# Performance work log

Measured on AMD Instinct MI355X. Metric: run time of the kernel, lower is better.

## Reference

```python
import jax, jax.numpy as jnp
import numpy as np

N = 50000
E = 800000
IN = 256
C = 64  # hidden_channels
H = 4   # heads
NEG_SLOPE = 0.2


def _rand(key, shape, scale=0.05):
    return jax.random.normal(key, shape, dtype=jnp.float32) * scale


def setup_inputs() -> dict:
    key = jax.random.key(0)
    ks = jax.random.split(key, 32)
    inp = {
        'x': jax.random.normal(ks[0], (N, IN), dtype=jnp.float32),
        'edge_index': jax.random.randint(ks[1], (2, E), 0, N, dtype=jnp.int64),
        'edge_attr': jax.random.uniform(ks[2], (E, 1), dtype=jnp.float32),
    }
    ki = 3
    for l, din in zip((1, 2, 3), (IN, C, C)):
        inp[f'Wl{l}'] = _rand(ks[ki + 0], (din, H * C))
        inp[f'bl{l}'] = jnp.zeros((H * C,), jnp.float32)
        inp[f'Wr{l}'] = _rand(ks[ki + 1], (din, H * C))
        inp[f'br{l}'] = jnp.zeros((H * C,), jnp.float32)
        inp[f'We{l}'] = _rand(ks[ki + 2], (1, H * C))
        inp[f'att{l}'] = _rand(ks[ki + 3], (H, C))
        inp[f'bias{l}'] = jnp.zeros((C,), jnp.float32)
        ki += 4
    inp['prelu_w'] = jnp.full((C,), 0.25, jnp.float32)  # nn.PReLU default init
    return inp


def gatv2_layer(x, src, dst, eattr, Wl, bl, Wr, br, We, att, bias, n):
    h, c = att.shape
    xl = (x @ Wl + bl).reshape(n, h, c)   # source transform
    xr = (x @ Wr + br).reshape(n, h, c)   # destination transform
    ee = (eattr @ We).reshape(-1, h, c)   # edge-feature transform
    m = xl[src] + xr[dst] + ee            # [E', H, C] per-edge messages
    score = jnp.sum(jax.nn.leaky_relu(m, NEG_SLOPE) * att, axis=-1)  # [E', H]
    # segment softmax over destination node neighborhoods (PyG softmax, eps=1e-16)
    mx = jax.ops.segment_max(score, dst, num_segments=n)
    mx = jnp.where(jnp.isfinite(mx), mx, 0.0)
    ex = jnp.exp(score - mx[dst])
    den = jax.ops.segment_sum(ex, dst, num_segments=n)
    alpha = ex / (den[dst] + 1e-16)
    out = jax.ops.segment_sum(alpha[:, :, None] * xl[src], dst, num_segments=n)
    return out.mean(axis=1) + bias        # concat=False -> head mean, then bias


def reference(x, edge_index, edge_attr,
              Wl1, bl1, Wr1, br1, We1, att1, bias1,
              Wl2, bl2, Wr2, br2, We2, att2, bias2,
              Wl3, bl3, Wr3, br3, We3, att3, bias3,
              prelu_w):
    src, dst = edge_index[0], edge_index[1]
    n = x.shape[0]
    # add_self_loops with fill_value='mean': self-loop attr = mean of incoming edge_attr
    cnt = jax.ops.segment_sum(jnp.ones((src.shape[0],), jnp.float32), dst, num_segments=n)
    loop_attr = jax.ops.segment_sum(edge_attr, dst, num_segments=n) / jnp.maximum(cnt, 1.0)[:, None]
    loops = jnp.arange(n, dtype=src.dtype)
    src2 = jnp.concatenate([src, loops])
    dst2 = jnp.concatenate([dst, loops])
    ea2 = jnp.concatenate([edge_attr, loop_attr], axis=0)

    h = gatv2_layer(x, src2, dst2, ea2, Wl1, bl1, Wr1, br1, We1, att1, bias1, n)
    h = gatv2_layer(h, src2, dst2, ea2, Wl2, bl2, Wr2, br2, We2, att2, bias2, n)
    h = gatv2_layer(h, src2, dst2, ea2, Wl3, bl3, Wr3, br3, We3, att3, bias3, n)
    return jnp.where(h >= 0, h, prelu_w * h)  # PReLU per-channel
```

## Files before the change

### kernel.cpp

```cpp
#include <hip/hip_runtime.h>

#define HC 256
#define CCH 64
#define NEG 0.2f

__device__ __forceinline__ float lk(float m) { return m > 0.f ? m : NEG * m; }


__global__ void deg_kernel(const int* __restrict__ dst,
                           const float* __restrict__ eattr,
                           int* __restrict__ cnt, float* __restrict__ sumf, int E) {
  int e = blockIdx.x * blockDim.x + threadIdx.x;
  if (e >= E) return;
  int d = dst[e];
  atomicAdd(&cnt[d], 1);
  atomicAdd(&sumf[d], eattr[e]);
}

__global__ void scan_kernel(const int* __restrict__ cnt, const float* __restrict__ sumf,
                            int* __restrict__ rowptr, float* __restrict__ loopat, int n) {
  __shared__ int wsum[16];
  __shared__ int carry_s;
  int tid = threadIdx.x, lane = tid & 63, w = tid >> 6;
  if (tid == 0) carry_s = 0;
  __syncthreads();
  for (int base = 0; base < n; base += 1024) {
    int i = base + tid;
    int v = (i < n) ? cnt[i] : 0;
    int s = v;
    #pragma unroll
    for (int off = 1; off < 64; off <<= 1) {
      int t = __shfl_up(s, off, 64);
      if (lane >= off) s += t;
    }
    if (lane == 63) wsum[w] = s;
    __syncthreads();
    int woff = 0;
    for (int j = 0; j < w; j++) woff += wsum[j];
    int excl = carry_s + woff + s - v;
    if (i < n) {
      rowptr[i] = excl;
      loopat[i] = sumf[i] / fmaxf((float)v, 1.0f);
    }
    __syncthreads();
    if (tid == 1023) carry_s = excl + v;
    __syncthreads();
  }
  if (threadIdx.x == 0) rowptr[n] = carry_s;
}

__global__ void csr_fill_kernel(const int* __restrict__ src,
                                const int* __restrict__ dst,
                                const float* __restrict__ eattr,
                                const int* __restrict__ rowptr,
                                int* __restrict__ fill,
                                int* __restrict__ csr_src, float* __restrict__ csr_ea, int E) {
  int e = blockIdx.x * blockDim.x + threadIdx.x;
  if (e >= E) return;
  int d = dst[e];
  int p = atomicAdd(&fill[d], 1);
  int slot = rowptr[d] + p;
  csr_src[slot] = src[e];
  csr_ea[slot] = eattr[e];
}


__global__ __launch_bounds__(256)
void gemm_dual(const float* __restrict__ A,
               const float* __restrict__ Wl, const float* __restrict__ bl,
               const float* __restrict__ Wr, const float* __restrict__ br,
               float* __restrict__ xl, float* __restrict__ xr,
               int nrows, int K) {
  __shared__ float As[16][132];
  __shared__ float Ws[16][64];
  const float* W; const float* bb; float* out; int bn;
  if (blockIdx.x < 4) { W = Wl; bb = bl; out = xl; bn = blockIdx.x * 64; }
  else                { W = Wr; bb = br; out = xr; bn = (blockIdx.x - 4) * 64; }
  int bm = blockIdx.y * 128;
  int tx = threadIdx.x & 15;
  int ty = threadIdx.x >> 4;
  int arow = threadIdx.x & 127;
  int akk  = (threadIdx.x >> 7) * 8;
  int wkk  = threadIdx.x >> 4;
  int wc4  = (threadIdx.x & 15) * 4;
  float acc[8][4] = {};
  int row0 = bm + arow;
  for (int k0 = 0; k0 < K; k0 += 16) {
    float4 a0 = make_float4(0.f,0.f,0.f,0.f), a1 = a0;
    if (row0 < nrows) {
      const float* ap = A + (size_t)row0 * K + k0 + akk;
      a0 = *(const float4*)ap;
      a1 = *(const float4*)(ap + 4);
    }
    As[akk+0][arow] = a0.x; As[akk+1][arow] = a0.y;
    As[akk+2][arow] = a0.z; As[akk+3][arow] = a0.w;
    As[akk+4][arow] = a1.x; As[akk+5][arow] = a1.y;
    As[akk+6][arow] = a1.z; As[akk+7][arow] = a1.w;
    *(float4*)&Ws[wkk][wc4] = *(const float4*)(W + (size_t)(k0 + wkk) * HC + bn + wc4);
    __syncthreads();
    #pragma unroll
    for (int k = 0; k < 16; k++) {
      float av[8], wv[4];
      *(float4*)&av[0] = *(const float4*)&As[k][ty * 8];
      *(float4*)&av[4] = *(const float4*)&As[k][ty * 8 + 4];
      *(float4*)&wv[0] = *(const float4*)&Ws[k][tx * 4];
      #pragma unroll
      for (int i = 0; i < 8; i++)
        #pragma unroll
        for (int j = 0; j < 4; j++)
          acc[i][j] = fmaf(av[i], wv[j], acc[i][j]);
    }
    __syncthreads();
  }
  float4 bv = *(const float4*)(bb + bn + tx * 4);
  #pragma unroll
  for (int i = 0; i < 8; i++) {
    int row = bm + ty * 8 + i;
    if (row < nrows) {
      float4 o;
      o.x = acc[i][0] + bv.x;
      o.y = acc[i][1] + bv.y;
      o.z = acc[i][2] + bv.z;
      o.w = acc[i][3] + bv.w;
      *(float4*)(out + (size_t)row * HC + bn + tx * 4) = o;
    }
  }
}


template<int B>
__device__ __forceinline__ void proc_edges(
    const float* __restrict__ xl, int i,
    const int* __restrict__ csr_src, const float* __restrict__ csr_ea,
    const float4 xr4, const float4 we4, const float4 ah4, int l4,
    float& mx, float& den, float4& acc) {
  int sn[B]; float ea[B]; float4 v[B]; float s[B];
  #pragma unroll
  for (int j = 0; j < B; j++) { sn[j] = csr_src[i + j]; ea[j] = csr_ea[i + j]; }
  #pragma unroll
  for (int j = 0; j < B; j++)
    v[j] = *(const float4*)(xl + (size_t)sn[j] * HC + l4);
  #pragma unroll
  for (int j = 0; j < B; j++) {
    float mx_ = fmaf(ea[j], we4.x, v[j].x + xr4.x);
    float my_ = fmaf(ea[j], we4.y, v[j].y + xr4.y);
    float mz_ = fmaf(ea[j], we4.z, v[j].z + xr4.z);
    float mw_ = fmaf(ea[j], we4.w, v[j].w + xr4.w);
    s[j] = lk(mx_) * ah4.x + lk(my_) * ah4.y + lk(mz_) * ah4.z + lk(mw_) * ah4.w;
  }
  #pragma unroll
  for (int off = 8; off >= 1; off >>= 1)
    #pragma unroll
    for (int j = 0; j < B; j++) s[j] += __shfl_xor(s[j], off, 64);
  float bm = s[0];
  #pragma unroll
  for (int j = 1; j < B; j++) bm = fmaxf(bm, s[j]);
  float newm = fmaxf(mx, bm);
  float r = __expf(mx - newm);
  den *= r; acc.x *= r; acc.y *= r; acc.z *= r; acc.w *= r;
  #pragma unroll
  for (int j = 0; j < B; j++) {
    float p = __expf(s[j] - newm);
    den += p;
    acc.x = fmaf(p, v[j].x, acc.x);
    acc.y = fmaf(p, v[j].y, acc.y);
    acc.z = fmaf(p, v[j].z, acc.z);
    acc.w = fmaf(p, v[j].w, acc.w);
  }
  mx = newm;
}

__global__ __launch_bounds__(256)
void gat_edge(const float* __restrict__ xl, const float* __restrict__ xr,
              const float* __restrict__ loopat, const int* __restrict__ rowptr,
              const int* __restrict__ csr_src, const float* __restrict__ csr_ea,
              const float* __restrict__ We, const float* __restrict__ att,
              const float* __restrict__ bias, const float* __restrict__ prelu_w,
              float* __restrict__ out, int n, int is_last) {
  int node = blockIdx.x;
  int l    = threadIdx.x & 63;
  int wv   = threadIdx.x >> 6;
  int l4   = l * 4;
  float4 we4 = *(const float4*)(We + l4);
  float4 ah4 = *(const float4*)(att + l4);
  float4 xr4 = *(const float4*)(xr + (size_t)node * HC + l4);

  float mx, den; float4 acc;
  if (wv == 0) {
    float4 vs = *(const float4*)(xl + (size_t)node * HC + l4);
    float la = loopat[node];
    float mx_ = fmaf(la, we4.x, vs.x + xr4.x);
    float my_ = fmaf(la, we4.y, vs.y + xr4.y);
    float mz_ = fmaf(la, we4.z, vs.z + xr4.z);
    float mw_ = fmaf(la, we4.w, vs.w + xr4.w);
    float t = lk(mx_) * ah4.x + lk(my_) * ah4.y + lk(mz_) * ah4.z + lk(mw_) * ah4.w;
    #pragma unroll
    for (int off = 8; off >= 1; off >>= 1) t += __shfl_xor(t, off, 64);
    mx = t; den = 1.f; acc = vs;
  } else {
    mx = -3.4e38f; den = 0.f; acc = make_float4(0.f, 0.f, 0.f, 0.f);
  }

  int beg = rowptr[node], end = rowptr[node + 1];
  int per = (end - beg + 3) >> 2;
  int wbeg = beg + wv * per;
  int wend = min(wbeg + per, end);
  int i = wbeg;
  for (; i + 4 <= wend; i += 4)
    proc_edges<4>(xl, i, csr_src, csr_ea, xr4, we4, ah4, l4, mx, den, acc);
  for (; i < wend; i++)
    proc_edges<1>(xl, i, csr_src, csr_ea, xr4, we4, ah4, l4, mx, den, acc);

  __shared__ float  s_mx[4][4];
  __shared__ float  s_den[4][4];
  __shared__ float4 s_acc[4][64];
  int h = l >> 4;
  s_acc[wv][l] = acc;
  if ((l & 15) == 0) { s_mx[wv][h] = mx; s_den[wv][h] = den; }
  __syncthreads();
  if (wv == 0) {
    float M = fmaxf(fmaxf(s_mx[0][h], s_mx[1][h]), fmaxf(s_mx[2][h], s_mx[3][h]));
    float dt = 0.f;
    float4 a = make_float4(0.f, 0.f, 0.f, 0.f);
    #pragma unroll
    for (int w = 0; w < 4; w++) {
      float f = __expf(s_mx[w][h] - M);
      dt = fmaf(s_den[w][h], f, dt);
      float4 aw = s_acc[w][l];
      a.x = fmaf(aw.x, f, a.x);
      a.y = fmaf(aw.y, f, a.y);
      a.z = fmaf(aw.z, f, a.z);
      a.w = fmaf(aw.w, f, a.w);
    }
    float inv = 1.f / (dt + 1e-16f);
    a.x *= inv; a.y *= inv; a.z *= inv; a.w *= inv;
    a.x += __shfl_xor(a.x, 16, 64); a.x += __shfl_xor(a.x, 32, 64);
    a.y += __shfl_xor(a.y, 16, 64); a.y += __shfl_xor(a.y, 32, 64);
    a.z += __shfl_xor(a.z, 16, 64); a.z += __shfl_xor(a.z, 32, 64);
    a.w += __shfl_xor(a.w, 16, 64); a.w += __shfl_xor(a.w, 32, 64);
    if (l < 16) {
      int c = l * 4;
      float4 bv = *(const float4*)(bias + c);
      float4 o;
      o.x = 0.25f * a.x + bv.x;
      o.y = 0.25f * a.y + bv.y;
      o.z = 0.25f * a.z + bv.z;
      o.w = 0.25f * a.w + bv.w;
      if (is_last) {
        float4 pw = *(const float4*)(prelu_w + c);
        o.x = o.x >= 0.f ? o.x : pw.x * o.x;
        o.y = o.y >= 0.f ? o.y : pw.y * o.y;
        o.z = o.z >= 0.f ? o.z : pw.z * o.z;
        o.w = o.w >= 0.f ? o.w : pw.w * o.w;
      }
      *(float4*)(out + (size_t)node * CCH + c) = o;
    }
  }
}


extern "C" void kernel_launch(void* const* d_in, const int* in_sizes, int n_in,
                              void* d_out, int out_size, void* d_ws, size_t ws_size,
                              hipStream_t stream) {
  const float* x     = (const float*)d_in[0];
  const int*   ei    = (const int*)d_in[1];
  const float* eattr = (const float*)d_in[2];
  int N = in_sizes[0] / HC;
  int E = in_sizes[1] / 2;
  const int* src = ei;
  const int* dst = ei + E;

  const float* Wl[3]  = {(const float*)d_in[3],  (const float*)d_in[10], (const float*)d_in[17]};
  const float* bl[3]  = {(const float*)d_in[4],  (const float*)d_in[11], (const float*)d_in[18]};
  const float* Wr[3]  = {(const float*)d_in[5],  (const float*)d_in[12], (const float*)d_in[19]};
  const float* br[3]  = {(const float*)d_in[6],  (const float*)d_in[13], (const float*)d_in[20]};
  const float* Wev[3] = {(const float*)d_in[7],  (const float*)d_in[14], (const float*)d_in[21]};
  const float* attv[3]= {(const float*)d_in[8],  (const float*)d_in[15], (const float*)d_in[22]};
  const float* bias[3]= {(const float*)d_in[9],  (const float*)d_in[16], (const float*)d_in[23]};
  const float* prelu  = (const float*)d_in[24];

  char* p = (char*)d_ws;
  float* xl     = (float*)p; p += (size_t)N * HC * 4;
  float* xr     = (float*)p; p += (size_t)N * HC * 4;
  float* hbuf   = (float*)p; p += (size_t)N * CCH * 4;
  int*   cnt    = (int*)p;   p += (size_t)N * 4;
  int*   fill   = (int*)p;   p += (size_t)N * 4;
  float* sumf   = (float*)p; p += (size_t)N * 4;
  float* loopat = (float*)p; p += (size_t)N * 4;
  int*   rowptr = (int*)p;   p += (size_t)(N + 8) * 4;
  int*   csr_src= (int*)p;   p += (size_t)E * 4;
  float* csr_ea = (float*)p; p += (size_t)E * 4;

  hipMemsetAsync(cnt, 0, (size_t)N * 3 * 4, stream);

  int tb = 256;
  deg_kernel<<<dim3((E + tb - 1) / tb), dim3(tb), 0, stream>>>(dst, eattr, cnt, sumf, E);
  scan_kernel<<<dim3(1), dim3(1024), 0, stream>>>(cnt, sumf, rowptr, loopat, N);
  csr_fill_kernel<<<dim3((E + tb - 1) / tb), dim3(tb), 0, stream>>>(src, dst, eattr, rowptr,
                                                                    fill, csr_src, csr_ea, E);

  const float* in = x;
  int K = 256;
  for (int l = 0; l < 3; l++) {
    dim3 g(8, (N + 127) / 128);
    gemm_dual<<<g, dim3(256), 0, stream>>>(in, Wl[l], bl[l], Wr[l], br[l], xl, xr, N, K);
    float* o = (l == 2) ? (float*)d_out : hbuf;
    gat_edge<<<dim3(N), dim3(256), 0, stream>>>(xl, xr, loopat, rowptr, csr_src, csr_ea,
                                                Wev[l], attv[l], bias[l], prelu, o, N, l == 2);
    in = hbuf;
    K = CCH;
  }
}
```

Measured before the change: 968.3 us.

## Parallelize CSR row-pointer scan and enlarge GEMM tile with register prefetch

The single-block serial scan over 50k nodes becomes a three-kernel multi-block scan: per-block scan, scan of block totals, then add the offsets back. The dual GEMM tile widens from 128x64 to 128x128, so each thread holds an 8x8 accumulator, A tiles are reloaded half as often, and the next k-slice is prefetched into registers while the current one is computed. The aim is to remove a latency-bound single-block launch and cut global/LDS traffic in the GEMM. The cost is two extra launches, and the larger accumulator raises register pressure under launch bounds (256,4).

```diff
diff --git a/kernel.cpp b/kernel.cpp
--- a/kernel.cpp
+++ b/kernel.cpp
@@ -17,36 +17,48 @@
   atomicAdd(&sumf[d], eattr[e]);
 }
 
-__global__ void scan_kernel(const int* __restrict__ cnt, const float* __restrict__ sumf,
-                            int* __restrict__ rowptr, float* __restrict__ loopat, int n) {
+__global__ __launch_bounds__(1024)
+void scanA(const int* __restrict__ cnt, const float* __restrict__ sumf,
+           int* __restrict__ rowptr, float* __restrict__ loopat,
+           int* __restrict__ btot, int n) {
   __shared__ int wsum[16];
-  __shared__ int carry_s;
   int tid = threadIdx.x, lane = tid & 63, w = tid >> 6;
-  if (tid == 0) carry_s = 0;
+  int i = blockIdx.x * 1024 + tid;
+  int v = (i < n) ? cnt[i] : 0;
+  int s = v;
+  #pragma unroll
+  for (int off = 1; off < 64; off <<= 1) {
+    int t = __shfl_up(s, off, 64);
+    if (lane >= off) s += t;
+  }
+  if (lane == 63) wsum[w] = s;
   __syncthreads();
-  for (int base = 0; base < n; base += 1024) {
-    int i = base + tid;
-    int v = (i < n) ? cnt[i] : 0;
-    int s = v;
-    #pragma unroll
-    for (int off = 1; off < 64; off <<= 1) {
-      int t = __shfl_up(s, off, 64);
-      if (lane >= off) s += t;
-    }
-    if (lane == 63) wsum[w] = s;
-    __syncthreads();
-    int woff = 0;
-    for (int j = 0; j < w; j++) woff += wsum[j];
-    int excl = carry_s + woff + s - v;
-    if (i < n) {
-      rowptr[i] = excl;
-      loopat[i] = sumf[i] / fmaxf((float)v, 1.0f);
-    }
-    __syncthreads();
-    if (tid == 1023) carry_s = excl + v;
-    __syncthreads();
-  }
-  if (threadIdx.x == 0) rowptr[n] = carry_s;
+  int woff = 0;
+  for (int j = 0; j < w; j++) woff += wsum[j];
+  if (i < n) {
+    rowptr[i] = woff + s - v;
+    loopat[i] = sumf[i] / fmaxf((float)v, 1.0f);
+  }
+  if (tid == 1023) btot[blockIdx.x] = woff + s;
+}
+
+__global__ void scanB(const int* __restrict__ btot, int* __restrict__ boff,
+                      int* __restrict__ rowptr_n, int nb) {
+  int lane = threadIdx.x;
+  int v = (lane < nb) ? btot[lane] : 0;
+  int s = v;
+  #pragma unroll
+  for (int off = 1; off < 64; off <<= 1) {
+    int t = __shfl_up(s, off, 64);
+    if (lane >= off) s += t;
+  }
+  if (lane < nb) boff[lane] = s - v;
+  if (lane == 63) *rowptr_n = s;
+}
+
+__global__ void scanC(int* __restrict__ rowptr, const int* __restrict__ boff, int n) {
+  int i = blockIdx.x * blockDim.x + threadIdx.x;
+  if (i < n) rowptr[i] += boff[i >> 10];
 }
 
 __global__ void csr_fill_kernel(const int* __restrict__ src,
@@ -65,64 +77,86 @@
 }
 
 
-__global__ __launch_bounds__(256)
-void gemm_dual(const float* __restrict__ A,
-               const float* __restrict__ Wl, const float* __restrict__ bl,
-               const float* __restrict__ Wr, const float* __restrict__ br,
-               float* __restrict__ xl, float* __restrict__ xr,
-               int nrows, int K) {
+__global__ __launch_bounds__(256, 4)
+void gemm128(const float* __restrict__ A,
+             const float* __restrict__ Wl, const float* __restrict__ bl,
+             const float* __restrict__ Wr, const float* __restrict__ br,
+             float* __restrict__ xl, float* __restrict__ xr,
+             int nrows, int K) {
   __shared__ float As[16][132];
-  __shared__ float Ws[16][64];
-  const float* W; const float* bb; float* out; int bn;
-  if (blockIdx.x < 4) { W = Wl; bb = bl; out = xl; bn = blockIdx.x * 64; }
-  else                { W = Wr; bb = br; out = xr; bn = (blockIdx.x - 4) * 64; }
+  __shared__ float Ws[16][132];
+  const float* W; const float* bb; float* out;
+  if (blockIdx.x < 2) { W = Wl; bb = bl; out = xl; }
+  else                { W = Wr; bb = br; out = xr; }
+  int bn = (blockIdx.x & 1) * 128;
   int bm = blockIdx.y * 128;
-  int tx = threadIdx.x & 15;
-  int ty = threadIdx.x >> 4;
-  int arow = threadIdx.x & 127;
-  int akk  = (threadIdx.x >> 7) * 8;
-  int wkk  = threadIdx.x >> 4;
-  int wc4  = (threadIdx.x & 15) * 4;
-  float acc[8][4] = {};
+  int tid = threadIdx.x;
+  int tx = tid & 15, ty = tid >> 4;
+  int arow = tid & 127;
+  int akk  = (tid >> 7) * 8;
+  int wkk  = tid >> 4;
+  int wc   = (tid & 15) * 4;
+
   int row0 = bm + arow;
-  for (int k0 = 0; k0 < K; k0 += 16) {
-    float4 a0 = make_float4(0.f,0.f,0.f,0.f), a1 = a0;
-    if (row0 < nrows) {
-      const float* ap = A + (size_t)row0 * K + k0 + akk;
-      a0 = *(const float4*)ap;
-      a1 = *(const float4*)(ap + 4);
-    }
+  bool aval = row0 < nrows;
+  const float* arp = A + (size_t)row0 * K + akk;
+  const float* wrp = W + (size_t)wkk * HC + bn + wc;
+
+  float4 z = make_float4(0.f, 0.f, 0.f, 0.f);
+  float4 a0 = aval ? *(const float4*)arp       : z;
+  float4 a1 = aval ? *(const float4*)(arp + 4) : z;
+  float4 w0 = *(const float4*)wrp;
+  float4 w1 = *(const float4*)(wrp + 64);
+
+  float acc[8][8] = {};
+  int k0 = 0;
+  while (true) {
     As[akk+0][arow] = a0.x; As[akk+1][arow] = a0.y;
     As[akk+2][arow] = a0.z; As[akk+3][arow] = a0.w;
     As[akk+4][arow] = a1.x; As[akk+5][arow] = a1.y;
     As[akk+6][arow] = a1.z; As[akk+7][arow] = a1.w;
-    *(float4*)&Ws[wkk][wc4] = *(const float4*)(W + (size_t)(k0 + wkk) * HC + bn + wc4);
+    *(float4*)&Ws[wkk][wc]      = w0;
+    *(float4*)&Ws[wkk][wc + 64] = w1;
     __syncthreads();
+    k0 += 16;
+    bool more = k0 < K;
+    if (more) {
+      a0 = aval ? *(const float4*)(arp + k0)     : z;
+      a1 = aval ? *(const float4*)(arp + k0 + 4) : z;
+      w0 = *(const float4*)(wrp + (size_t)k0 * HC);
+      w1 = *(const float4*)(wrp + (size_t)k0 * HC + 64);
+    }
     #pragma unroll
     for (int k = 0; k < 16; k++) {
-      float av[8], wv[4];
+      float av[8], wv[8];
       *(float4*)&av[0] = *(const float4*)&As[k][ty * 8];
       *(float4*)&av[4] = *(const float4*)&As[k][ty * 8 + 4];
       *(float4*)&wv[0] = *(const float4*)&Ws[k][tx * 4];
+      *(float4*)&wv[4] = *(const float4*)&Ws[k][tx * 4 + 64];
       #pragma unroll
       for (int i = 0; i < 8; i++)
         #pragma unroll
-        for (int j = 0; j < 4; j++)
+        for (int j = 0; j < 8; j++)
           acc[i][j] = fmaf(av[i], wv[j], acc[i][j]);
     }
+    if (!more) break;
     __syncthreads();
   }
-  float4 bv = *(const float4*)(bb + bn + tx * 4);
+
+  float4 bv0 = *(const float4*)(bb + bn + tx * 4);
+  float4 bv1 = *(const float4*)(bb + bn + tx * 4 + 64);
   #pragma unroll
   for (int i = 0; i < 8; i++) {
     int row = bm + ty * 8 + i;
     if (row < nrows) {
-      float4 o;
-      o.x = acc[i][0] + bv.x;
-      o.y = acc[i][1] + bv.y;
-      o.z = acc[i][2] + bv.z;
-      o.w = acc[i][3] + bv.w;
-      *(float4*)(out + (size_t)row * HC + bn + tx * 4) = o;
+      float* op = out + (size_t)row * HC + bn + tx * 4;
+      float4 o0, o1;
+      o0.x = acc[i][0] + bv0.x; o0.y = acc[i][1] + bv0.y;
+      o0.z = acc[i][2] + bv0.z; o0.w = acc[i][3] + bv0.w;
+      o1.x = acc[i][4] + bv1.x; o1.y = acc[i][5] + bv1.y;
+      o1.z = acc[i][6] + bv1.z; o1.w = acc[i][7] + bv1.w;
+      *(float4*)op        = o0;
+      *(float4*)(op + 64) = o1;
     }
   }
 }
@@ -288,22 +322,27 @@
   float* sumf   = (float*)p; p += (size_t)N * 4;
   float* loopat = (float*)p; p += (size_t)N * 4;
   int*   rowptr = (int*)p;   p += (size_t)(N + 8) * 4;
+  int*   btot   = (int*)p;   p += 64 * 4;
+  int*   boff   = (int*)p;   p += 64 * 4;
   int*   csr_src= (int*)p;   p += (size_t)E * 4;
   float* csr_ea = (float*)p; p += (size_t)E * 4;
 
   hipMemsetAsync(cnt, 0, (size_t)N * 3 * 4, stream);
 
   int tb = 256;
+  int nb = (N + 1023) / 1024;
   deg_kernel<<<dim3((E + tb - 1) / tb), dim3(tb), 0, stream>>>(dst, eattr, cnt, sumf, E);
-  scan_kernel<<<dim3(1), dim3(1024), 0, stream>>>(cnt, sumf, rowptr, loopat, N);
+  scanA<<<dim3(nb), dim3(1024), 0, stream>>>(cnt, sumf, rowptr, loopat, btot, N);
+  scanB<<<dim3(1), dim3(64), 0, stream>>>(btot, boff, rowptr + N, nb);
+  scanC<<<dim3((N + tb - 1) / tb), dim3(tb), 0, stream>>>(rowptr, boff, N);
   csr_fill_kernel<<<dim3((E + tb - 1) / tb), dim3(tb), 0, stream>>>(src, dst, eattr, rowptr,
                                                                     fill, csr_src, csr_ea, E);
 
   const float* in = x;
   int K = 256;
   for (int l = 0; l < 3; l++) {
-    dim3 g(8, (N + 127) / 128);
-    gemm_dual<<<g, dim3(256), 0, stream>>>(in, Wl[l], bl[l], Wr[l], br[l], xl, xr, N, K);
+    dim3 g(4, (N + 127) / 128);
+    gemm128<<<g, dim3(256), 0, stream>>>(in, Wl[l], bl[l], Wr[l], br[l], xl, xr, N, K);
     float* o = (l == 2) ? (float*)d_out : hbuf;
     gat_edge<<<dim3(N), dim3(256), 0, stream>>>(xl, xr, loopat, rowptr, csr_src, csr_ea,
                                                 Wev[l], attv[l], bias[l], prelu, o, N, l == 2);
```

Measured after the change: 1.206 ms. 24.6% more time.
